# Kernel tuning notes

Hardware: AMD Instinct MI355X
Metric: run time of the kernel (lower is better)

Reference implementation:

```python
import jax, jax.numpy as jnp
import numpy as np


def _f_map(x):
    # alpha = ||x||; x normalized; append a constant-1 feature
    alpha = jnp.linalg.norm(x, axis=-1, keepdims=True)
    xn = x / jnp.maximum(alpha, 1e-12)
    ones = jnp.ones(x.shape[:-1] + (1,), x.dtype)
    return jnp.concatenate([(1.0 - 0.5 ** alpha) * xn, ones], axis=-1)


def _mh_lka(q, k, v):
    # kernelized linear attention: cumsum of k (x) v outer products along seq
    q = _f_map(q)  # (B, N, D+1)
    k = _f_map(k)
    kv = jnp.cumsum(jnp.einsum('bnd,bne->bnde', k, v), axis=1)  # (B,N,D+1,D)
    k_ = jnp.cumsum(k, axis=1)
    qk = jnp.einsum('bnd,bnd->bn', q, k_)[..., None]
    qkv = jnp.einsum('bnd,bnde->bne', q, kv)
    return qkv / qk


def _lstm(x, Wih, Whh, bih, bhh):
    # single-layer batch-first LSTM, torch gate order (i, f, g, o)
    B, H = x.shape[0], Whh.shape[1]
    bias = bih + bhh
    def step(carry, xt):
        h, c = carry
        g = xt @ Wih.T + h @ Whh.T + bias  # (B, 4H)
        i, f, gg, o = jnp.split(g, 4, axis=-1)
        c = jax.nn.sigmoid(f) * c + jax.nn.sigmoid(i) * jnp.tanh(gg)
        h = jax.nn.sigmoid(o) * jnp.tanh(c)
        return (h, c), h
    h0 = jnp.zeros((B, H), x.dtype)
    c0 = jnp.zeros((B, H), x.dtype)
    _, hs = jax.lax.scan(step, (h0, c0), x.transpose(1, 0, 2))
    return hs.transpose(1, 0, 2)


def setup_inputs() -> dict:
    in_sz, hid, n_h, out_sz = 512, 64, 8, 512
    B, N = 2, 2048
    key = jax.random.key(0)
    ks = jax.random.split(key, 10)
    s = 0.02
    f32 = jnp.float32
    return {
        'x': jax.random.normal(ks[0], (B, N, in_sz), f32),
        'Wq': jax.random.normal(ks[1], (in_sz, hid * n_h), f32) * s,
        'bq': jnp.zeros((hid * n_h,), f32),
        'Wk': jax.random.normal(ks[2], (in_sz, hid * n_h), f32) * s,
        'bk': jnp.zeros((hid * n_h,), f32),
        'Wv': jax.random.normal(ks[3], (in_sz, hid * n_h), f32) * s,
        'bv': jnp.zeros((hid * n_h,), f32),
        'Wih': jax.random.normal(ks[4], (4 * hid, hid), f32) * s,
        'Whh': jax.random.normal(ks[5], (4 * hid, hid), f32) * s,
        'bih': jnp.zeros((4 * hid,), f32),
        'bhh': jnp.zeros((4 * hid,), f32),
        'W1': jax.random.normal(ks[6], (hid * n_h, out_sz), f32) * s,
        'b1': jnp.zeros((out_sz,), f32),
        'W2': jax.random.normal(ks[7], (out_sz, out_sz), f32) * s,
        'b2': jnp.zeros((out_sz,), f32),
        'gamma': jnp.ones((out_sz,), f32),
        'beta': jnp.zeros((out_sz,), f32),
    }


def reference(x, Wq, bq, Wk, bk, Wv, bv, Wih, Whh, bih, bhh, W1, b1, W2, b2, gamma, beta):
    B, N, _ = x.shape
    H = Whh.shape[1]
    n_h = Wq.shape[1] // H
    def proj(W, b_):
        y = x @ W + b_                              # (B, N, n_h*H)
        return y.reshape(B, N, n_h, H).transpose(0, 2, 1, 3).reshape(B * n_h, N, H)
    q, k, v = proj(Wq, bq), proj(Wk, bk), proj(Wv, bv)
    o = _mh_lka(q, k, v)                            # (B*n_h, N, H)
    o = o + _lstm(o, Wih, Whh, bih, bhh)
    o = o.reshape(B, n_h, N, H).transpose(0, 2, 1, 3).reshape(B, N, n_h * H)
    o = jax.nn.gelu(o @ W1 + b1, approximate=False) @ W2 + b2
    mu = o.mean(-1, keepdims=True)
    var = o.var(-1, keepdims=True)
    return (o - mu) / jnp.sqrt(var + 1e-5) * gamma + beta
```

## Files before the change

kernel.cpp:

```cpp
#include <hip/hip_runtime.h>
#include <hip/hip_bf16.h>
#include <hip/hip_fp16.h>

using bf16 = __hip_bfloat16;
using ushort_t = unsigned short;
using uint32 = unsigned int;
typedef _Float16 f16x2 __attribute__((ext_vector_type(2)));
typedef short short8 __attribute__((ext_vector_type(8)));
typedef float floatx4 __attribute__((ext_vector_type(4)));

__device__ __forceinline__ float u2f(ushort_t u) {
  return __uint_as_float(((unsigned int)u) << 16);
}
__device__ __forceinline__ bool probe_f32(const void* graw) {
  return ((const ushort_t*)graw)[0] != 0x3F80;
}
__device__ __forceinline__ float scrub(float v) {
  return fminf(fmaxf(v, -1e4f), 1e4f);
}
__device__ __forceinline__ short f2b(float x) {
  uint32 u = __float_as_uint(x);
  return (short)((u + 0x7FFFu + ((u >> 16) & 1u)) >> 16);
}
__device__ __forceinline__ float frcp(float x) {
#if __has_builtin(__builtin_amdgcn_rcpf)
  return __builtin_amdgcn_rcpf(x);
#else
  return 1.f / x;
#endif
}
__device__ __forceinline__ float fexp2(float x) {
#if __has_builtin(__builtin_amdgcn_exp2f)
  return __builtin_amdgcn_exp2f(x);
#else
  return exp2f(x);
#endif
}
template<int CTRL>
__device__ __forceinline__ float qperm(float x) {
  return __int_as_float(__builtin_amdgcn_mov_dpp(__float_as_int(x), CTRL, 0xF, 0xF, false));
}
__device__ __forceinline__ float fdot2(uint32 a, uint32 b, float c) {
#if __has_builtin(__builtin_amdgcn_fdot2)
  return __builtin_amdgcn_fdot2(__builtin_bit_cast(f16x2, a),
                                __builtin_bit_cast(f16x2, b), c, false);
#else
  const f16x2 av = __builtin_bit_cast(f16x2, a);
  const f16x2 bv = __builtin_bit_cast(f16x2, b);
  return c + (float)av[0] * (float)bv[0] + (float)av[1] * (float)bv[1];
#endif
}

#define LSTM_S1 -1.4426950408889634f
#define LSTM_S2 -2.8853900817779268f

struct Ptrs { const void* p[16]; };

__global__ __launch_bounds__(256) void cvt_k(Ptrs ps, float* __restrict__ dst) {
  const int sizes[16] = {262144,512,262144,512,262144,512,16384,16384,
                         256,256,262144,512,262144,512,512,512};
  int idx = blockIdx.x * 256 + threadIdx.x;
  if (idx >= 1347840) return;
  const bool f32in = probe_f32(ps.p[14]);
  if (idx >= 1347584) {
    const int i = idx - 1347584;
    float a, b;
    if (f32in) { a = ((const float*)ps.p[8])[i]; b = ((const float*)ps.p[9])[i]; }
    else { a = u2f(((const ushort_t*)ps.p[8])[i]); b = u2f(((const ushort_t*)ps.p[9])[i]); }
    dst[idx] = a + b;
    return;
  }
  int seg = 0, off = idx;
  while (off >= sizes[seg]) { off -= sizes[seg]; seg++; }
  float v;
  if (f32in) v = ((const float*)ps.p[seg])[off];
  else       v = u2f(((const ushort_t*)ps.p[seg])[off]);
  dst[idx] = v;
}

template<int AMODE, int ACT, int BMODE, int OUT>
__global__ __launch_bounds__(256) void gemm_mfma(
    const void* __restrict__ A, const float* __restrict__ B,
    const float* __restrict__ bias, const void* __restrict__ graw,
    void* __restrict__ Cv, int M, int N, int K)
{
  __shared__ __align__(16) short As2[64][36];
  __shared__ __align__(16) short Bs2[64][36];
  const int t = threadIdx.x;
  const int row0 = blockIdx.y * 64, col0 = blockIdx.x * 64;
  const int w = t >> 6, lane = t & 63;
  const int quad = lane >> 4, lr = lane & 15;
  bool f32in = true;
  if (AMODE == 1) f32in = probe_f32(graw);

  const int am = t >> 2, akq = t & 3;
  const int bn = t & 63, bkq = t >> 6;

  floatx4 acc[4] = {{0,0,0,0},{0,0,0,0},{0,0,0,0},{0,0,0,0}};

  for (int k0 = 0; k0 < K; k0 += 32) {
    {
      const size_t aoff = (size_t)(row0 + am) * K + (k0 + akq * 8);
      short8 ap;
      if (AMODE == 0 || f32in) {
        const float4 v0 = *reinterpret_cast<const float4*>((const float*)A + aoff);
        const float4 v1 = *reinterpret_cast<const float4*>((const float*)A + aoff + 4);
        ap[0]=f2b(v0.x); ap[1]=f2b(v0.y); ap[2]=f2b(v0.z); ap[3]=f2b(v0.w);
        ap[4]=f2b(v1.x); ap[5]=f2b(v1.y); ap[6]=f2b(v1.z); ap[7]=f2b(v1.w);
      } else {
        const ushort4 u0 = *reinterpret_cast<const ushort4*>((const ushort_t*)A + aoff);
        const ushort4 u1 = *reinterpret_cast<const ushort4*>((const ushort_t*)A + aoff + 4);
        ap[0]=(short)u0.x; ap[1]=(short)u0.y; ap[2]=(short)u0.z; ap[3]=(short)u0.w;
        ap[4]=(short)u1.x; ap[5]=(short)u1.y; ap[6]=(short)u1.z; ap[7]=(short)u1.w;
      }
      *reinterpret_cast<short8*>(&As2[am][akq * 8]) = ap;
    }
    {
      short8 bpk;
      if (BMODE == 0) {
        const float* bp = B + (size_t)(k0 + bkq * 8) * N + col0 + bn;
        #pragma unroll
        for (int j = 0; j < 8; j++) bpk[j] = f2b(bp[(size_t)j * N]);
      } else {
        const float* bp = B + (size_t)(col0 + bn) * K + k0 + bkq * 8;
        const float4 v0 = *reinterpret_cast<const float4*>(bp);
        const float4 v1 = *reinterpret_cast<const float4*>(bp + 4);
        bpk[0]=f2b(v0.x); bpk[1]=f2b(v0.y); bpk[2]=f2b(v0.z); bpk[3]=f2b(v0.w);
        bpk[4]=f2b(v1.x); bpk[5]=f2b(v1.y); bpk[6]=f2b(v1.z); bpk[7]=f2b(v1.w);
      }
      *reinterpret_cast<short8*>(&Bs2[bn][bkq * 8]) = bpk;
    }
    __syncthreads();
    {
      const short8 af = *reinterpret_cast<const short8*>(&As2[w * 16 + lr][quad * 8]);
      #pragma unroll
      for (int ct = 0; ct < 4; ct++) {
        const short8 bf = *reinterpret_cast<const short8*>(&Bs2[ct * 16 + lr][quad * 8]);
        acc[ct] = __builtin_amdgcn_mfma_f32_16x16x32_bf16(af, bf, acc[ct], 0, 0, 0);
      }
    }
    __syncthreads();
  }
  #pragma unroll
  for (int ct = 0; ct < 4; ct++) {
    const int col = col0 + ct * 16 + lr;
    const float bb = bias[col];
    #pragma unroll
    for (int r = 0; r < 4; r++) {
      const int row = row0 + w * 16 + quad * 4 + r;
      float v = acc[ct][r] + bb;
      if (ACT == 1) v = 0.5f * v * (1.0f + erff(v * 0.70710678118654752f));
      if (ACT == 2) v *= ((col >> 6) == 2) ? LSTM_S2 : LSTM_S1;
      if (OUT == 0) ((float*)Cv)[(size_t)row * N + col] = scrub(v);
      else ((__half*)Cv)[(size_t)row * N + col] = __float2half(scrub(v));
    }
  }
}

__global__ __launch_bounds__(256) void qkv_mfma(
    const void* __restrict__ A, const float* __restrict__ cvtBase,
    const void* __restrict__ graw, float* __restrict__ wsBase)
{
  const int M = 4096, N = 512, K = 512;
  __shared__ __align__(16) short As2[64][36];
  __shared__ __align__(16) short Bs2[64][36];
  const int t = threadIdx.x;
  const int sel = blockIdx.x >> 3;
  const float* B = cvtBase + (size_t)sel * 262656;
  const float* bias = cvtBase + 262144 + (size_t)sel * 262656;
  float* C = wsBase + (size_t)sel * 2097152;
  const int row0 = blockIdx.y * 64, col0 = (blockIdx.x & 7) * 64;
  const int w = t >> 6, lane = t & 63;
  const int quad = lane >> 4, lr = lane & 15;
  const bool f32in = probe_f32(graw);

  const int am = t >> 2, akq = t & 3;
  const int bn = t & 63, bkq = t >> 6;

  floatx4 acc[4] = {{0,0,0,0},{0,0,0,0},{0,0,0,0},{0,0,0,0}};

  for (int k0 = 0; k0 < K; k0 += 32) {
    {
      const size_t aoff = (size_t)(row0 + am) * K + (k0 + akq * 8);
      short8 ap;
      if (f32in) {
        const float4 v0 = *reinterpret_cast<const float4*>((const float*)A + aoff);
        const float4 v1 = *reinterpret_cast<const float4*>((const float*)A + aoff + 4);
        ap[0]=f2b(v0.x); ap[1]=f2b(v0.y); ap[2]=f2b(v0.z); ap[3]=f2b(v0.w);
        ap[4]=f2b(v1.x); ap[5]=f2b(v1.y); ap[6]=f2b(v1.z); ap[7]=f2b(v1.w);
      } else {
        const ushort4 u0 = *reinterpret_cast<const ushort4*>((const ushort_t*)A + aoff);
        const ushort4 u1 = *reinterpret_cast<const ushort4*>((const ushort_t*)A + aoff + 4);
        ap[0]=(short)u0.x; ap[1]=(short)u0.y; ap[2]=(short)u0.z; ap[3]=(short)u0.w;
        ap[4]=(short)u1.x; ap[5]=(short)u1.y; ap[6]=(short)u1.z; ap[7]=(short)u1.w;
      }
      *reinterpret_cast<short8*>(&As2[am][akq * 8]) = ap;
    }
    {
      const float* bp = B + (size_t)(k0 + bkq * 8) * N + col0 + bn;
      short8 bpk;
      #pragma unroll
      for (int j = 0; j < 8; j++) bpk[j] = f2b(bp[(size_t)j * N]);
      *reinterpret_cast<short8*>(&Bs2[bn][bkq * 8]) = bpk;
    }
    __syncthreads();
    {
      const short8 af = *reinterpret_cast<const short8*>(&As2[w * 16 + lr][quad * 8]);
      #pragma unroll
      for (int ct = 0; ct < 4; ct++) {
        const short8 bf = *reinterpret_cast<const short8*>(&Bs2[ct * 16 + lr][quad * 8]);
        acc[ct] = __builtin_amdgcn_mfma_f32_16x16x32_bf16(af, bf, acc[ct], 0, 0, 0);
      }
    }
    __syncthreads();
  }
  #pragma unroll
  for (int ct = 0; ct < 4; ct++) {
    const int col = col0 + ct * 16 + lr;
    const float bb = bias[col];
    #pragma unroll
    for (int r = 0; r < 4; r++) {
      const int row = row0 + w * 16 + quad * 4 + r;
      C[(size_t)row * N + col] = scrub(acc[ct][r] + bb);
    }
  }
}

__global__ __launch_bounds__(256) void attn_pass1(
    const float* __restrict__ kb, const float* __restrict__ vb,
    float* __restrict__ S, float* __restrict__ kcS)
{
  const int c = blockIdx.x, bh = blockIdx.y;
  const int b = bh >> 3, hd = bh & 7;
  const int t = threadIdx.x;
  const int e = t & 63, p = t >> 6;

  __shared__ __align__(16) float kf_s[64][64];
  __shared__ __align__(16) float v_s[64][64];

  for (int r = 0; r < 16; r++) {
    const int nl = p * 16 + r;
    const size_t base = ((size_t)(b * 2048 + c * 64 + nl)) * 512 + hd * 64 + e;
    const float kr = kb[base];
    const float vr = vb[base];
    float s = kr * kr;
    #pragma unroll
    for (int off = 32; off > 0; off >>= 1) s += __shfl_xor(s, off);
    const float ak = sqrtf(s);
    kf_s[nl][e] = (1.0f - exp2f(-ak)) * frcp(fmaxf(ak, 1e-12f)) * kr;
    v_s[nl][e] = vr;
  }
  __syncthreads();

  float Sl[16], kcl[16], S64 = 0.f;
  #pragma unroll
  for (int i = 0; i < 16; i++) { Sl[i] = 0.f; kcl[i] = 0.f; }
  for (int nn = 0; nn < 64; nn++) {
    const float ve = v_s[nn][e];
    #pragma unroll
    for (int i = 0; i < 16; i++) {
      const float kfd = kf_s[nn][p * 16 + i];
      Sl[i]  += kfd * ve;
      kcl[i] += kfd;
    }
    if (p == 0) S64 += ve;
  }
  const size_t sbase = ((size_t)(bh * 32 + c)) * 4160;
  #pragma unroll
  for (int i = 0; i < 16; i++) S[sbase + (p * 16 + i) * 64 + e] = Sl[i];
  if (p == 0) S[sbase + 4096 + e] = S64;
  if (e == 0) {
    const size_t kbase = ((size_t)(bh * 32 + c)) * 64;
    #pragma unroll
    for (int i = 0; i < 16; i++) kcS[kbase + p * 16 + i] = kcl[i];
  }
}

__global__ __launch_bounds__(256) void attn_pass2(
    float* __restrict__ S, float* __restrict__ kcS)
{
  const int bh = blockIdx.y;
  const int idx = blockIdx.x * 256 + threadIdx.x;
  if (idx < 4160) {
    const size_t base = (size_t)bh * 32 * 4160 + idx;
    float v[32];
    #pragma unroll
    for (int cc = 0; cc < 32; cc++) v[cc] = S[base + (size_t)cc * 4160];
    float run = 0.f;
    #pragma unroll
    for (int cc = 0; cc < 32; cc++) { const float tmp = v[cc]; v[cc] = run; run += tmp; }
    #pragma unroll
    for (int cc = 0; cc < 32; cc++) S[base + (size_t)cc * 4160] = v[cc];
  }
  if (blockIdx.x == 0 && threadIdx.x < 64) {
    const size_t base = (size_t)bh * 32 * 64 + threadIdx.x;
    float v[32];
    #pragma unroll
    for (int cc = 0; cc < 32; cc++) v[cc] = kcS[base + (size_t)cc * 64];
    float run = 0.f;
    #pragma unroll
    for (int cc = 0; cc < 32; cc++) { const float tmp = v[cc]; v[cc] = run; run += tmp; }
    #pragma unroll
    for (int cc = 0; cc < 32; cc++) kcS[base + (size_t)cc * 64] = v[cc];
  }
}

__global__ __launch_bounds__(256) void attn_pass3(
    const float* __restrict__ qb, const float* __restrict__ kb, const float* __restrict__ vb,
    const float* __restrict__ S, const float* __restrict__ kcS,
    float* __restrict__ ao)
{
  const int c = blockIdx.x, bh = blockIdx.y;
  const int b = bh >> 3, hd = bh & 7;
  const int t = threadIdx.x;
  const int e = t & 63, p = t >> 6;

  __shared__ __align__(16) float qf_s[64][64], kf_s[64][64], v_s[64][64];
  __shared__ __align__(16) float accp_s[2][4][64];
  __shared__ float qkp_s[2][4];

  for (int r = 0; r < 16; r++) {
    const int nl = p * 16 + r;
    const size_t base = ((size_t)(b * 2048 + c * 64 + nl)) * 512 + hd * 64 + e;
    const float qr = qb[base];
    const float kr = kb[base];
    const float vr = vb[base];
    float sq = qr * qr, sk = kr * kr;
    #pragma unroll
    for (int off = 32; off > 0; off >>= 1) {
      sq += __shfl_xor(sq, off);
      sk += __shfl_xor(sk, off);
    }
    const float aq = sqrtf(sq), ak = sqrtf(sk);
    qf_s[nl][e] = (1.0f - exp2f(-aq)) * frcp(fmaxf(aq, 1e-12f)) * qr;
    kf_s[nl][e] = (1.0f - exp2f(-ak)) * frcp(fmaxf(ak, 1e-12f)) * kr;
    v_s[nl][e] = vr;
  }

  float Sl[16], kcl[16], S64;
  {
    const size_t sbase = ((size_t)(bh * 32 + c)) * 4160;
    #pragma unroll
    for (int i = 0; i < 16; i++) Sl[i] = S[sbase + (p * 16 + i) * 64 + e];
    S64 = S[sbase + 4096 + e];
    const size_t kbase = ((size_t)(bh * 32 + c)) * 64;
    #pragma unroll
    for (int i = 0; i < 16; i++) kcl[i] = kcS[kbase + p * 16 + i];
  }
  __syncthreads();

  for (int nn = 0; nn < 64; nn++) {
    const int n = c * 64 + nn;
    const int buf = nn & 1;
    const float ve = v_s[nn][e];
    float accp = 0.f, qkp = 0.f;
    #pragma unroll
    for (int i = 0; i < 16; i++) {
      const float kfd = kf_s[nn][p * 16 + i];
      const float qfd = qf_s[nn][p * 16 + i];
      Sl[i]  += kfd * ve;
      accp   += qfd * Sl[i];
      kcl[i] += kfd;
      qkp    += qfd * kcl[i];
    }
    if (p == 0) {
      S64  += ve;
      accp += S64;
      qkp  += (float)(n + 1);
    }
    accp_s[buf][p][e] = accp;
    if (e == 0) qkp_s[buf][p] = qkp;
    __syncthreads();
    if (t < 64) {
      const float num = accp_s[buf][0][t] + accp_s[buf][1][t] +
                        accp_s[buf][2][t] + accp_s[buf][3][t];
      float den = qkp_s[buf][0] + qkp_s[buf][1] + qkp_s[buf][2] + qkp_s[buf][3];
      den = fmaxf(den, 1e-6f);
      ao[((size_t)(bh * 2048 + n)) * 64 + t] = scrub(num / den);
    }
  }
}

__global__ __attribute__((amdgpu_flat_work_group_size(256, 256), amdgpu_waves_per_eu(1, 1)))
void lstm_k(
    const float* __restrict__ ao, const __half* __restrict__ G,
    const float* __restrict__ Whhf, float* __restrict__ y1)
{
  const int bh = blockIdx.x;
  const int b = bh >> 3, hd = bh & 7;
  const int t = threadIdx.x;
  const int gate = t & 3;
  const int e = t >> 2;
  const int jg = gate * 64 + e;
  const bool isG = (gate == 2);
  const bool owner = (gate == 0);

  __shared__ __align__(16) _Float16 hh[2][64];

  uint32 w[32];
  {
    const float ws = isG ? LSTM_S2 : LSTM_S1;
    const float4* wp = reinterpret_cast<const float4*>(Whhf + (size_t)jg * 64);
    #pragma unroll
    for (int i = 0; i < 16; i++) {
      const float4 v = wp[i];
      f16x2 p0; p0[0] = (_Float16)(v.x * ws); p0[1] = (_Float16)(v.y * ws);
      f16x2 p1; p1[0] = (_Float16)(v.z * ws); p1[1] = (_Float16)(v.w * ws);
      w[i * 2 + 0] = __builtin_bit_cast(uint32, p0);
      w[i * 2 + 1] = __builtin_bit_cast(uint32, p1);
    }
  }
  #pragma unroll
  for (int i = 0; i < 32; i++) asm volatile("" : "+v"(w[i]));

  float c = 0.f;
  if (t < 64) hh[0][t] = (_Float16)0.f;

  const size_t aobase = (size_t)bh * 2048 * 64;
  const size_t gbase  = (size_t)bh * 2048 * 256;
  const ushort_t* Gu = reinterpret_cast<const ushort_t*>(G);

  float gcur[16], aoc[16];
  {
    #pragma unroll
    for (int j = 0; j < 16; j++) {
      const ushort_t gu = Gu[gbase + (size_t)j * 256 + jg];
      gcur[j] = (float)__builtin_bit_cast(_Float16, gu);
      aoc[j] = ao[aobase + (size_t)j * 64 + e];
    }
  }
  __syncthreads();

  for (int ch = 0; ch < 128; ch++) {
    ushort_t gn2[16]; float aon[16];
    if (ch + 1 < 128) {
      #pragma unroll
      for (int j = 0; j < 16; j++) {
        gn2[j] = Gu[gbase + (size_t)(ch + 1) * 4096 + (size_t)j * 256 + jg];
        aon[j] = ao[aobase + (size_t)(ch + 1) * 1024 + (size_t)j * 64 + e];
      }
    }
    #pragma unroll
    for (int nn = 0; nn < 16; nn++) {
      const int n = ch * 16 + nn;
      const int hb = n & 1;
      const float gin = gcur[nn];
      const uint4* hp = reinterpret_cast<const uint4*>(&hh[hb][0]);
      float d0 = 0.f, d1 = 0.f, d2 = 0.f, d3 = 0.f;
      #pragma unroll
      for (int q = 0; q < 8; q++) {
        const uint4 h4 = hp[q];
        d0 = fdot2(w[q * 4 + 0], h4.x, d0);
        d1 = fdot2(w[q * 4 + 1], h4.y, d1);
        d2 = fdot2(w[q * 4 + 2], h4.z, d2);
        d3 = fdot2(w[q * 4 + 3], h4.w, d3);
      }
      const float arg = gin + (d0 + d1) + (d2 + d3);
      const float e2 = fexp2(arg);
      const float sg = frcp(1.0f + e2);
      const float act = isG ? __builtin_fmaf(sg, 5.7707801635558536f, LSTM_S2) : sg;
      const float af  = qperm<0xB1>(act);
      const float ag  = qperm<0x4E>(act);
      const float ao4 = qperm<0x1B>(act);
      if (owner) {
        c = __builtin_fmaf(af, c, act * ag);
        const float ex = fexp2(c);
        const float tc = __builtin_fmaf(-2.0f, frcp(ex + 1.0f), 1.0f);
        const float h = ao4 * tc;
        hh[1 - hb][e] = (_Float16)h;
        y1[((size_t)(b * 2048 + n)) * 512 + hd * 64 + e] =
            scrub(aoc[nn] + h);
      }
      if (nn == 15 && ch + 1 < 128) {
        #pragma unroll
        for (int j = 0; j < 16; j++) {
          gcur[j] = (float)__builtin_bit_cast(_Float16, gn2[j]);
          aoc[j] = aon[j];
        }
      }
      asm volatile("s_waitcnt lgkmcnt(0)\n\ts_barrier" ::: "memory");
    }
  }
}

__global__ __launch_bounds__(256) void ln_k(
    const float* __restrict__ X, const float* __restrict__ gamf,
    const float* __restrict__ betf, const void* __restrict__ graw,
    void* __restrict__ out)
{
  const int r = blockIdx.x;
  const int t = threadIdx.x;
  const bool f32out = probe_f32(graw);
  const float a = X[(size_t)r * 512 + t];
  const float b = X[(size_t)r * 512 + 256 + t];
  float s1 = a + b, s2 = a * a + b * b;
  #pragma unroll
  for (int off = 32; off > 0; off >>= 1) {
    s1 += __shfl_xor(s1, off);
    s2 += __shfl_xor(s2, off);
  }
  __shared__ float sh1[4], sh2[4];
  if ((t & 63) == 0) { sh1[t >> 6] = s1; sh2[t >> 6] = s2; }
  __syncthreads();
  const float tot1 = sh1[0] + sh1[1] + sh1[2] + sh1[3];
  const float tot2 = sh2[0] + sh2[1] + sh2[2] + sh2[3];
  const float mu = tot1 * (1.0f / 512.0f);
  const float var = fmaxf(tot2 * (1.0f / 512.0f) - mu * mu, 0.f);
  const float rs = rsqrtf(var + 1e-5f);
  const float o0 = scrub((a - mu) * rs * gamf[t]       + betf[t]);
  const float o1 = scrub((b - mu) * rs * gamf[256 + t] + betf[256 + t]);
  if (f32out) {
    ((float*)out)[(size_t)r * 512 + t]       = o0;
    ((float*)out)[(size_t)r * 512 + 256 + t] = o1;
  } else {
    ((bf16*)out)[(size_t)r * 512 + t]       = __float2bfloat16(o0);
    ((bf16*)out)[(size_t)r * 512 + 256 + t] = __float2bfloat16(o1);
  }
}

extern "C" void kernel_launch(void* const* d_in, const int* in_sizes, int n_in,
                              void* d_out, int out_size, void* d_ws, size_t ws_size,
                              hipStream_t stream) {
  const void* x    = d_in[0];
  const void* graw = d_in[15];

  float* ws  = (float*)d_ws;
  float* q   = ws;
  float* kb  = q   + 2097152;
  float* v   = kb  + 2097152;
  float* ao  = v   + 2097152;
  float* S   = ao  + 2097152;
  float* kcS = S   + 2129920;
  float* cvt = kcS + 32768;
  float* Wihf = cvt + 787968;   float* Whhf = cvt + 804352;
  float* W1f  = cvt + 821248;   float* b1f  = cvt + 1083392;
  float* W2f  = cvt + 1083904;  float* b2f_ = cvt + 1346048;
  float* gamf = cvt + 1346560;  float* betf = cvt + 1347072;
  float* bsum = cvt + 1347584;
  __half* G = (__half*)kb;
  float* y1 = q;
  float* f1 = kb;
  float* f2 = v;

  Ptrs ps;
  for (int i = 0; i < 16; i++) ps.p[i] = d_in[i + 1];

  cvt_k<<<(1347840 + 255) / 256, 256, 0, stream>>>(ps, cvt);

  qkv_mfma<<<dim3(24, 64), 256, 0, stream>>>(x, cvt, graw, ws);
  attn_pass1<<<dim3(32, 16), 256, 0, stream>>>(kb, v, S, kcS);
  attn_pass2<<<dim3(17, 16), 256, 0, stream>>>(S, kcS);
  attn_pass3<<<dim3(32, 16), 256, 0, stream>>>(q, kb, v, S, kcS, ao);
  gemm_mfma<0, 2, 1, 1><<<dim3(4, 512), 256, 0, stream>>>(ao, Wihf, bsum, graw, G, 32768, 256, 64);
  lstm_k<<<16, 256, 0, stream>>>(ao, G, Whhf, y1);
  gemm_mfma<0, 1, 0, 0><<<dim3(8, 64), 256, 0, stream>>>(y1, W1f, b1f, graw, f1, 4096, 512, 512);
  gemm_mfma<0, 0, 0, 0><<<dim3(8, 64), 256, 0, stream>>>(f1, W2f, b2f_, graw, f2, 4096, 512, 512);
  ln_k<<<4096, 256, 0, stream>>>(f2, gamf, betf, graw, d_out);
}
```

Measured before the change: 887.2 us.

## Run LSTM recurrence in one wave per sequence, computing all gates per lane

The LSTM kernel shrinks from four waves, where lanes split the four gates and exchange results through DPP and a block barrier every timestep, to a single 64-lane wave. Each lane now holds all four gate weight rows (128 packed registers) and computes every gate itself. Because there is only one wave, the per-step barrier and the cross-lane shuffles go away, and the hidden state uses a single LDS buffer. A large dummy LDS allocation forces one block per CU. The trade-off is four times as many serial dot-product instructions per lane per step on the critical recurrence path, plus much higher register pressure.

```diff
diff --git a/kernel.cpp b/kernel.cpp
--- a/kernel.cpp
+++ b/kernel.cpp
@@ -35,10 +35,6 @@
 #else
   return exp2f(x);
 #endif
-}
-template<int CTRL>
-__device__ __forceinline__ float qperm(float x) {
-  return __int_as_float(__builtin_amdgcn_mov_dpp(__float_as_int(x), CTRL, 0xF, 0xF, false));
 }
 __device__ __forceinline__ float fdot2(uint32 a, uint32 b, float c) {
 #if __has_builtin(__builtin_amdgcn_fdot2)
@@ -381,104 +377,104 @@
   }
 }
 
-__global__ __attribute__((amdgpu_flat_work_group_size(256, 256), amdgpu_waves_per_eu(1, 1)))
+__global__ __attribute__((amdgpu_flat_work_group_size(64, 64), amdgpu_waves_per_eu(1, 1)))
 void lstm_k(
     const float* __restrict__ ao, const __half* __restrict__ G,
     const float* __restrict__ Whhf, float* __restrict__ y1)
 {
   const int bh = blockIdx.x;
   const int b = bh >> 3, hd = bh & 7;
-  const int t = threadIdx.x;
-  const int gate = t & 3;
-  const int e = t >> 2;
-  const int jg = gate * 64 + e;
-  const bool isG = (gate == 2);
-  const bool owner = (gate == 0);
-
-  __shared__ __align__(16) _Float16 hh[2][64];
-
-  uint32 w[32];
-  {
-    const float ws = isG ? LSTM_S2 : LSTM_S1;
-    const float4* wp = reinterpret_cast<const float4*>(Whhf + (size_t)jg * 64);
+  const int e = threadIdx.x;
+
+  __shared__ __align__(16) _Float16 hh[64];
+  __shared__ char lds_spread[81920];
+
+  uint32 w[128];
+  #pragma unroll
+  for (int g = 0; g < 4; g++) {
+    const float ws = (g == 2) ? LSTM_S2 : LSTM_S1;
+    const float4* wp = reinterpret_cast<const float4*>(Whhf + (size_t)(g * 64 + e) * 64);
     #pragma unroll
     for (int i = 0; i < 16; i++) {
       const float4 v = wp[i];
       f16x2 p0; p0[0] = (_Float16)(v.x * ws); p0[1] = (_Float16)(v.y * ws);
       f16x2 p1; p1[0] = (_Float16)(v.z * ws); p1[1] = (_Float16)(v.w * ws);
-      w[i * 2 + 0] = __builtin_bit_cast(uint32, p0);
-      w[i * 2 + 1] = __builtin_bit_cast(uint32, p1);
-    }
-  }
-  #pragma unroll
-  for (int i = 0; i < 32; i++) asm volatile("" : "+v"(w[i]));
+      w[g * 32 + i * 2 + 0] = __builtin_bit_cast(uint32, p0);
+      w[g * 32 + i * 2 + 1] = __builtin_bit_cast(uint32, p1);
+    }
+  }
+  #pragma unroll
+  for (int i = 0; i < 128; i++) asm volatile("" : "+v"(w[i]));
+
+  if (G == (const __half*)(size_t)1) ((volatile char*)lds_spread)[0] = 1;
 
   float c = 0.f;
-  if (t < 64) hh[0][t] = (_Float16)0.f;
-
-  const size_t aobase = (size_t)bh * 2048 * 64;
-  const size_t gbase  = (size_t)bh * 2048 * 256;
+  hh[e] = (_Float16)0.f;
+
+  const size_t aobase = (size_t)bh * 2048 * 64 + e;
+  const size_t gbase  = (size_t)bh * 2048 * 256 + e;
+  const size_t ybase  = ((size_t)b * 2048) * 512 + hd * 64 + e;
   const ushort_t* Gu = reinterpret_cast<const ushort_t*>(G);
 
-  float gcur[16], aoc[16];
-  {
-    #pragma unroll
-    for (int j = 0; j < 16; j++) {
-      const ushort_t gu = Gu[gbase + (size_t)j * 256 + jg];
-      gcur[j] = (float)__builtin_bit_cast(_Float16, gu);
-      aoc[j] = ao[aobase + (size_t)j * 64 + e];
-    }
-  }
-  __syncthreads();
-
-  for (int ch = 0; ch < 128; ch++) {
-    ushort_t gn2[16]; float aon[16];
-    if (ch + 1 < 128) {
+  uint32 gcu[16]; float aoc[4];
+  #pragma unroll
+  for (int j = 0; j < 4; j++) {
+    #pragma unroll
+    for (int g = 0; g < 4; g++)
+      gcu[j * 4 + g] = Gu[gbase + (size_t)j * 256 + g * 64];
+    aoc[j] = ao[aobase + (size_t)j * 64];
+  }
+
+  for (int ch = 0; ch < 512; ch++) {
+    uint32 gn[16]; float aon[4];
+    if (ch + 1 < 512) {
       #pragma unroll
-      for (int j = 0; j < 16; j++) {
-        gn2[j] = Gu[gbase + (size_t)(ch + 1) * 4096 + (size_t)j * 256 + jg];
-        aon[j] = ao[aobase + (size_t)(ch + 1) * 1024 + (size_t)j * 64 + e];
-      }
-    }
-    #pragma unroll
-    for (int nn = 0; nn < 16; nn++) {
-      const int n = ch * 16 + nn;
-      const int hb = n & 1;
-      const float gin = gcur[nn];
-      const uint4* hp = reinterpret_cast<const uint4*>(&hh[hb][0]);
-      float d0 = 0.f, d1 = 0.f, d2 = 0.f, d3 = 0.f;
+      for (int j = 0; j < 4; j++) {
+        #pragma unroll
+        for (int g = 0; g < 4; g++)
+          gn[j * 4 + g] = Gu[gbase + (size_t)(ch * 4 + 4 + j) * 256 + g * 64];
+        aon[j] = ao[aobase + (size_t)(ch * 4 + 4 + j) * 64];
+      }
+    }
+    #pragma unroll
+    for (int nn = 0; nn < 4; nn++) {
+      const int n = ch * 4 + nn;
+      const uint4* hp = reinterpret_cast<const uint4*>(&hh[0]);
+      float aI = 0.f, bI = 0.f, aF = 0.f, bF = 0.f;
+      float aG = 0.f, bG = 0.f, aO = 0.f, bO = 0.f;
       #pragma unroll
       for (int q = 0; q < 8; q++) {
         const uint4 h4 = hp[q];
-        d0 = fdot2(w[q * 4 + 0], h4.x, d0);
-        d1 = fdot2(w[q * 4 + 1], h4.y, d1);
-        d2 = fdot2(w[q * 4 + 2], h4.z, d2);
-        d3 = fdot2(w[q * 4 + 3], h4.w, d3);
-      }
-      const float arg = gin + (d0 + d1) + (d2 + d3);
-      const float e2 = fexp2(arg);
-      const float sg = frcp(1.0f + e2);
-      const float act = isG ? __builtin_fmaf(sg, 5.7707801635558536f, LSTM_S2) : sg;
-      const float af  = qperm<0xB1>(act);
-      const float ag  = qperm<0x4E>(act);
-      const float ao4 = qperm<0x1B>(act);
-      if (owner) {
-        c = __builtin_fmaf(af, c, act * ag);
-        const float ex = fexp2(c);
-        const float tc = __builtin_fmaf(-2.0f, frcp(ex + 1.0f), 1.0f);
-        const float h = ao4 * tc;
-        hh[1 - hb][e] = (_Float16)h;
-        y1[((size_t)(b * 2048 + n)) * 512 + hd * 64 + e] =
-            scrub(aoc[nn] + h);
-      }
-      if (nn == 15 && ch + 1 < 128) {
+        aI = fdot2(w[  0 + q*4 + 0], h4.x, aI); bI = fdot2(w[  0 + q*4 + 1], h4.y, bI);
+        aI = fdot2(w[  0 + q*4 + 2], h4.z, aI); bI = fdot2(w[  0 + q*4 + 3], h4.w, bI);
+        aF = fdot2(w[ 32 + q*4 + 0], h4.x, aF); bF = fdot2(w[ 32 + q*4 + 1], h4.y, bF);
+        aF = fdot2(w[ 32 + q*4 + 2], h4.z, aF); bF = fdot2(w[ 32 + q*4 + 3], h4.w, bF);
+        aG = fdot2(w[ 64 + q*4 + 0], h4.x, aG); bG = fdot2(w[ 64 + q*4 + 1], h4.y, bG);
+        aG = fdot2(w[ 64 + q*4 + 2], h4.z, aG); bG = fdot2(w[ 64 + q*4 + 3], h4.w, bG);
+        aO = fdot2(w[ 96 + q*4 + 0], h4.x, aO); bO = fdot2(w[ 96 + q*4 + 1], h4.y, bO);
+        aO = fdot2(w[ 96 + q*4 + 2], h4.z, aO); bO = fdot2(w[ 96 + q*4 + 3], h4.w, bO);
+      }
+      const float gI = (float)__builtin_bit_cast(_Float16, (ushort_t)gcu[nn*4 + 0]);
+      const float gF = (float)__builtin_bit_cast(_Float16, (ushort_t)gcu[nn*4 + 1]);
+      const float gG = (float)__builtin_bit_cast(_Float16, (ushort_t)gcu[nn*4 + 2]);
+      const float gO = (float)__builtin_bit_cast(_Float16, (ushort_t)gcu[nn*4 + 3]);
+      const float sI = frcp(1.0f + fexp2(gI + (aI + bI)));
+      const float sF = frcp(1.0f + fexp2(gF + (aF + bF)));
+      const float sG = frcp(1.0f + fexp2(gG + (aG + bG)));
+      const float sO = frcp(1.0f + fexp2(gO + (aO + bO)));
+      const float gAct = __builtin_fmaf(sG, 5.7707801635558536f, LSTM_S2);
+      c = __builtin_fmaf(sF, c, sI * gAct);
+      const float ex = fexp2(c);
+      const float tc = __builtin_fmaf(-2.0f, frcp(ex + 1.0f), 1.0f);
+      const float h = sO * tc;
+      hh[e] = (_Float16)h;
+      y1[ybase + (size_t)n * 512] = scrub(aoc[nn] + h);
+      if (nn == 3 && ch + 1 < 512) {
         #pragma unroll
-        for (int j = 0; j < 16; j++) {
-          gcur[j] = (float)__builtin_bit_cast(_Float16, gn2[j]);
-          aoc[j] = aon[j];
-        }
-      }
-      asm volatile("s_waitcnt lgkmcnt(0)\n\ts_barrier" ::: "memory");
+        for (int j = 0; j < 16; j++) gcu[j] = gn[j];
+        #pragma unroll
+        for (int j = 0; j < 4; j++) aoc[j] = aon[j];
+      }
     }
   }
 }
@@ -552,7 +548,7 @@
   attn_pass2<<<dim3(17, 16), 256, 0, stream>>>(S, kcS);
   attn_pass3<<<dim3(32, 16), 256, 0, stream>>>(q, kb, v, S, kcS, ao);
   gemm_mfma<0, 2, 1, 1><<<dim3(4, 512), 256, 0, stream>>>(ao, Wihf, bsum, graw, G, 32768, 256, 64);
-  lstm_k<<<16, 256, 0, stream>>>(ao, G, Whhf, y1);
+  lstm_k<<<16, 64, 0, stream>>>(ao, G, Whhf, y1);
   gemm_mfma<0, 1, 0, 0><<<dim3(8, 64), 256, 0, stream>>>(y1, W1f, b1f, graw, f1, 4096, 512, 512);
   gemm_mfma<0, 0, 0, 0><<<dim3(8, 64), 256, 0, stream>>>(f1, W2f, b2f_, graw, f2, 4096, 512, 512);
   ln_k<<<4096, 256, 0, stream>>>(f2, gamf, betf, graw, d_out);
```

New measurement: 1.064 ms. +20.0%, slower.
